# Performance work log

Hardware: AMD Instinct MI355X
Metric: run time of the kernel (lower is better)

Reference implementation:

```python
import jax, jax.numpy as jnp
import numpy as np

N_USER = 100000
N_ITEM = 100000
E = 500000
EMB, HID, OUT = 128, 128, 64


def _mean_agg(msg_src, src, dst, n_dst):
    """Gather per-edge messages from src nodes, segment-mean onto dst nodes."""
    m = msg_src[src]  # [E, d]
    s = jax.ops.segment_sum(m, dst, num_segments=n_dst)
    cnt = jax.ops.segment_sum(jnp.ones((src.shape[0],), m.dtype), dst,
                              num_segments=n_dst)
    # DGL mean reducer yields 0 for nodes with no in-edges
    return jnp.where(cnt[:, None] > 0, s / jnp.maximum(cnt, 1.0)[:, None], 0.0)


def _layer(feat_u, feat_i, W0, b0, Wui, bui, Wiu, biu,
           src_ui, dst_ui, src_iu, dst_iu):
    # shared self-transform (weight0) -> residual h0 on every ntype
    h0_u = feat_u @ W0 + b0
    h0_i = feat_i @ W0 + b0
    # per-etype transform of source features
    wh_u = feat_u @ Wui + bui  # messages along user->item
    wh_i = feat_i @ Wiu + biu  # messages along item->user
    h_i = _mean_agg(wh_u, src_ui, dst_ui, N_ITEM) + h0_i
    h_u = _mean_agg(wh_i, src_iu, dst_iu, N_USER) + h0_u
    return h_u, h_i


def setup_inputs() -> dict:
    key = jax.random.key(0)
    ks = jax.random.split(key, 12)
    sc_e = 1.0 / np.sqrt(EMB)
    sc_h = 1.0 / np.sqrt(HID)
    return {
        "emb_user": jax.random.normal(ks[0], (N_USER, EMB), jnp.float32),
        "emb_item": jax.random.normal(ks[1], (N_ITEM, EMB), jnp.float32),
        "W1_0": jax.random.normal(ks[2], (EMB, HID), jnp.float32) * sc_e,
        "b1_0": jnp.zeros((HID,), jnp.float32),
        "W1_ui": jax.random.normal(ks[3], (EMB, HID), jnp.float32) * sc_e,
        "b1_ui": jnp.zeros((HID,), jnp.float32),
        "W1_iu": jax.random.normal(ks[4], (EMB, HID), jnp.float32) * sc_e,
        "b1_iu": jnp.zeros((HID,), jnp.float32),
        "W2_0": jax.random.normal(ks[5], (HID, OUT), jnp.float32) * sc_h,
        "b2_0": jnp.zeros((OUT,), jnp.float32),
        "W2_ui": jax.random.normal(ks[6], (HID, OUT), jnp.float32) * sc_h,
        "b2_ui": jnp.zeros((OUT,), jnp.float32),
        "W2_iu": jax.random.normal(ks[7], (HID, OUT), jnp.float32) * sc_h,
        "b2_iu": jnp.zeros((OUT,), jnp.float32),
        "src_ui": jax.random.randint(ks[8], (E,), 0, N_USER, jnp.int32),
        "dst_ui": jax.random.randint(ks[9], (E,), 0, N_ITEM, jnp.int32),
        "src_iu": jax.random.randint(ks[10], (E,), 0, N_ITEM, jnp.int32),
        "dst_iu": jax.random.randint(ks[11], (E,), 0, N_USER, jnp.int32),
    }


def reference(emb_user, emb_item,
              W1_0, b1_0, W1_ui, b1_ui, W1_iu, b1_iu,
              W2_0, b2_0, W2_ui, b2_ui, W2_iu, b2_iu,
              src_ui, dst_ui, src_iu, dst_iu):
    h_u, h_i = _layer(emb_user, emb_item, W1_0, b1_0, W1_ui, b1_ui,
                      W1_iu, b1_iu, src_ui, dst_ui, src_iu, dst_iu)
    h_u = jax.nn.leaky_relu(h_u, 0.01)  # torch F.leaky_relu default slope
    h_i = jax.nn.leaky_relu(h_i, 0.01)
    h_u, h_i = _layer(h_u, h_i, W2_0, b2_0, W2_ui, b2_ui,
                      W2_iu, b2_iu, src_ui, dst_ui, src_iu, dst_iu)
    return h_u, h_i
```

## Files before the change

kernel.cpp:

```cpp
#include <hip/hip_runtime.h>

#define N_USER 100000
#define N_ITEM 100000
#define NEDGE  500000
#define CURS   100032
#define RCAP   16

#define B_FILL 978
#define B_CONV 12500
#define B_WT   384
#define B_TOT  (B_FILL + B_CONV + B_WT)

typedef __attribute__((ext_vector_type(8))) short short8;
typedef __attribute__((ext_vector_type(4))) float f32x4;

__device__ __forceinline__ unsigned short f2bf(float f) {
  union { float f; unsigned int u; } x{f};
  unsigned int r = x.u + 0x7fffu + ((x.u >> 16) & 1u);
  return (unsigned short)(r >> 16);
}
__device__ __forceinline__ float bf2f(unsigned short u) {
  union { unsigned int u; float f; } x{(unsigned int)u << 16};
  return x.f;
}

__global__ __launch_bounds__(256) void setup_k(
    const int* __restrict__ src_ui, const int* __restrict__ dst_ui,
    int* __restrict__ cur_i, int* __restrict__ csr_ui,
    const int* __restrict__ src_iu, const int* __restrict__ dst_iu,
    int* __restrict__ cur_u, int* __restrict__ csr_iu,
    const float* __restrict__ emb_u, const float* __restrict__ emb_i,
    unsigned short* __restrict__ ebu, unsigned short* __restrict__ ebi,
    const float* __restrict__ W10, const float* __restrict__ W1ui,
    const float* __restrict__ W1iu, const float* __restrict__ W20,
    const float* __restrict__ W2ui, const float* __restrict__ W2iu,
    unsigned short* __restrict__ WT1i, unsigned short* __restrict__ WT1u,
    unsigned short* __restrict__ WT2i, unsigned short* __restrict__ WT2u) {
  int b = (int)(((unsigned long long)blockIdx.x * 7919ull) % (unsigned long long)B_TOT);
  int tid = threadIdx.x;
  if (b < B_FILL) {
    const int *src, *dst; int *cur, *csr;
    int bb = b;
    if (bb < 489) { src = src_ui; dst = dst_ui; cur = cur_i; csr = csr_ui; }
    else { bb -= 489; src = src_iu; dst = dst_iu; cur = cur_u; csr = csr_iu; }
    int e0 = bb * 1024 + tid;
    int d[4], s[4];
    bool ok[4];
#pragma unroll
    for (int k = 0; k < 4; ++k) {
      int e = e0 + k * 256;
      ok[k] = (e < NEDGE);
      d[k] = ok[k] ? dst[e] : 0;
      s[k] = ok[k] ? src[e] : 0;
    }
    int p[4];
#pragma unroll
    for (int k = 0; k < 4; ++k) {
      int rk = (tid + k) & 3;
      p[k] = ok[k] ? atomicAdd(&cur[rk * CURS + d[k]], 1) : RCAP;
    }
#pragma unroll
    for (int k = 0; k < 4; ++k) {
      int rk = (tid + k) & 3;
      if (ok[k] && p[k] < RCAP)
        __builtin_nontemporal_store(s[k], &csr[d[k] * 64 + rk * RCAP + p[k]]);
    }
  } else if (b < B_FILL + B_CONV) {
    int blk = b - B_FILL;
    const float* src; unsigned short* dstp;
    if (blk < 6250) { src = emb_u; dstp = ebu; }
    else { blk -= 6250; src = emb_i; dstp = ebi; }
    size_t g = (size_t)blk * 2048 + (size_t)tid * 8;
    float4 x = *(const float4*)(src + g);
    float4 y = *(const float4*)(src + g + 4);
    short8 v{(short)f2bf(x.x), (short)f2bf(x.y), (short)f2bf(x.z), (short)f2bf(x.w),
             (short)f2bf(y.x), (short)f2bf(y.y), (short)f2bf(y.z), (short)f2bf(y.w)};
    *(short8*)(dstp + g) = v;
  } else {
    int t = (b - B_FILL - B_CONV) * 256 + tid;
    if (t < 32768) {
      int n = t >> 8, k = t & 255;
      float v = (k < 128) ? W10[k * 128 + n] : W1ui[(k - 128) * 128 + n];
      WT1i[t] = f2bf(v);
    } else if (t < 65536) {
      int q = t - 32768; int n = q >> 8, k = q & 255;
      float v = (k < 128) ? W10[k * 128 + n] : W1iu[(k - 128) * 128 + n];
      WT1u[q] = f2bf(v);
    } else if (t < 81920) {
      int q = t - 65536; int n = q >> 8, k = q & 255;
      float v = (k < 128) ? W20[k * 64 + n] : W2ui[(k - 128) * 64 + n];
      WT2i[q] = f2bf(v);
    } else {
      int q = t - 81920; int n = q >> 8, k = q & 255;
      float v = (k < 128) ? W20[k * 64 + n] : W2iu[(k - 128) * 64 + n];
      WT2u[q] = f2bf(v);
    }
  }
}

__global__ __launch_bounds__(256) void aggc_k(
    const unsigned short* __restrict__ featA, const int* __restrict__ curA,
    const int* __restrict__ csrA, unsigned short* __restrict__ outA,
    const unsigned short* __restrict__ featB, const int* __restrict__ curB,
    const int* __restrict__ csrB, unsigned short* __restrict__ outB,
    int nbA) {
  __shared__ int sidx[16][64];
  int b = blockIdx.x;
  const unsigned short* feat; const int* cur; const int* csr; unsigned short* out;
  if (b < nbA) { feat = featA; cur = curA; csr = csrA; out = outA; }
  else { b -= nbA; feat = featB; cur = curB; csr = csrB; out = outB; }
  int grp = threadIdx.x >> 4;
  int ln  = threadIdx.x & 15;
  int node = b * 16 + grp;

  int4 sl = *(const int4*)(csr + (size_t)node * 64 + ln * 4);
  int cr = cur[(size_t)(ln >> 2) * CURS + node];
  cr = min(cr, RCAP);
  int m = cr - (ln & 3) * 4;
  m = m < 0 ? 0 : (m > 4 ? 4 : m);
  int pre = m;
#pragma unroll
  for (int d = 1; d < 16; d <<= 1) {
    int t = __shfl_up(pre, d, 16);
    if (ln >= d) pre += t;
  }
  int start = pre - m;
  int deg = __shfl(pre, 15, 16);
  if (m > 0) sidx[grp][start] = sl.x;
  if (m > 1) sidx[grp][start + 1] = sl.y;
  if (m > 2) sidx[grp][start + 2] = sl.z;
  if (m > 3) sidx[grp][start + 3] = sl.w;
  __syncthreads();

  const int* lidx = sidx[grp];
  float a[8] = {0, 0, 0, 0, 0, 0, 0, 0};
  int j = 0;
  if (j + 4 <= deg) {
    int i0 = lidx[0], i1 = lidx[1], i2 = lidx[2], i3 = lidx[3];
    for (;;) {
      bool more = (j + 8 <= deg);
      int n0, n1, n2, n3;
      if (more) { n0 = lidx[j + 4]; n1 = lidx[j + 5]; n2 = lidx[j + 6]; n3 = lidx[j + 7]; }
      short8 v0 = *(const short8*)(feat + (size_t)i0 * 128 + ln * 8);
      short8 v1 = *(const short8*)(feat + (size_t)i1 * 128 + ln * 8);
      short8 v2 = *(const short8*)(feat + (size_t)i2 * 128 + ln * 8);
      short8 v3 = *(const short8*)(feat + (size_t)i3 * 128 + ln * 8);
#pragma unroll
      for (int d = 0; d < 8; ++d)
        a[d] += (bf2f((unsigned short)v0[d]) + bf2f((unsigned short)v1[d])) +
                (bf2f((unsigned short)v2[d]) + bf2f((unsigned short)v3[d]));
      j += 4;
      if (!more) break;
      i0 = n0; i1 = n1; i2 = n2; i3 = n3;
    }
  }
  if (j + 2 <= deg) {
    int i0 = lidx[j], i1 = lidx[j + 1];
    short8 v0 = *(const short8*)(feat + (size_t)i0 * 128 + ln * 8);
    short8 v1 = *(const short8*)(feat + (size_t)i1 * 128 + ln * 8);
#pragma unroll
    for (int d = 0; d < 8; ++d)
      a[d] += bf2f((unsigned short)v0[d]) + bf2f((unsigned short)v1[d]);
    j += 2;
  }
  if (j < deg) {
    short8 v = *(const short8*)(feat + (size_t)lidx[j] * 128 + ln * 8);
#pragma unroll
    for (int d = 0; d < 8; ++d) a[d] += bf2f((unsigned short)v[d]);
  }
  float sc = deg ? 1.f / (float)deg : 0.f;
  short8 pk;
#pragma unroll
  for (int d = 0; d < 8; ++d) pk[d] = (short)f2bf(a[d] * sc);
  *(short8*)(out + (size_t)node * 128 + ln * 8) = pk;
}

template <int N, bool LRELU, bool OUTBF16>
__global__ __launch_bounds__(256) void gemm2_k(
    const unsigned short* __restrict__ A1a, const unsigned short* __restrict__ A2a,
    const unsigned short* __restrict__ WTa, const float* __restrict__ b0a,
    const float* __restrict__ bea, const int* __restrict__ cura,
    void* __restrict__ outa,
    const unsigned short* __restrict__ A1b, const unsigned short* __restrict__ A2b,
    const unsigned short* __restrict__ WTb, const float* __restrict__ b0b,
    const float* __restrict__ beb, const int* __restrict__ curb,
    void* __restrict__ outb, int M, int nbA) {
  constexpr int BM = 64;
  constexpr int CPW = N / 4;
  constexpr int NCF = CPW / 16;
  __shared__ short As[BM * 128];
  __shared__ short Ws[N * 128];
  __shared__ float degmask[BM];

  int blk = blockIdx.x;
  const unsigned short* A1; const unsigned short* A2; const unsigned short* WT;
  const float* b0; const float* be; const int* cur; void* outv;
  if (blk < nbA) { A1 = A1a; A2 = A2a; WT = WTa; b0 = b0a; be = bea; cur = cura; outv = outa; }
  else { blk -= nbA; A1 = A1b; A2 = A2b; WT = WTb; b0 = b0b; be = beb; cur = curb; outv = outb; }

  const int tid = threadIdx.x;
  const int lane = tid & 63;
  const int wave = tid >> 6;
  const int row0 = blk * BM;
  const int colbase = wave * CPW;

  if (tid < BM) {
    int r = row0 + tid;
    int ds = 0;
    if (r < M)
      ds = cur[r] + cur[CURS + r] + cur[2 * CURS + r] + cur[3 * CURS + r];
    degmask[tid] = (ds > 0) ? 1.f : 0.f;
  }

  f32x4 acc[4][NCF] = {};

#pragma unroll
  for (int kh = 0; kh < 2; ++kh) {
    __syncthreads();
    const unsigned short* base = (kh == 0) ? A1 : A2;
#pragma unroll
    for (int it = 0; it < 4; ++it) {
      int chunk = tid + it * 256;
      int row = chunk >> 4, c16 = chunk & 15;
      int gr = row0 + row; if (gr > M - 1) gr = M - 1;
      short8 v = *(const short8*)(base + (size_t)gr * 128 + c16 * 8);
      int byteoff = row * 256 + ((c16 * 16) ^ ((row & 7) << 4));
      *(short8*)((char*)As + byteoff) = v;
    }
#pragma unroll
    for (int it = 0; it < (N * 16) / 256; ++it) {
      int chunk = tid + it * 256;
      int n = chunk >> 4, c16 = chunk & 15;
      short8 v = *(const short8*)(WT + (size_t)n * 256 + kh * 128 + c16 * 8);
      int byteoff = n * 256 + ((c16 * 16) ^ ((n & 7) << 4));
      *(short8*)((char*)Ws + byteoff) = v;
    }
    __syncthreads();

#pragma unroll
    for (int ks = 0; ks < 4; ++ks) {
      short8 af[4];
#pragma unroll
      for (int rf = 0; rf < 4; ++rf) {
        int row = rf * 16 + (lane & 15);
        int c16 = ks * 4 + (lane >> 4);
        int byteoff = row * 256 + ((c16 * 16) ^ ((row & 7) << 4));
        af[rf] = *(const short8*)((const char*)As + byteoff);
      }
      short8 wf[NCF];
#pragma unroll
      for (int cf = 0; cf < NCF; ++cf) {
        int n = colbase + cf * 16 + (lane & 15);
        int c16 = ks * 4 + (lane >> 4);
        int byteoff = n * 256 + ((c16 * 16) ^ ((n & 7) << 4));
        wf[cf] = *(const short8*)((const char*)Ws + byteoff);
      }
#pragma unroll
      for (int rf = 0; rf < 4; ++rf)
#pragma unroll
        for (int cf = 0; cf < NCF; ++cf)
          acc[rf][cf] = __builtin_amdgcn_mfma_f32_16x16x32_bf16(
              af[rf], wf[cf], acc[rf][cf], 0, 0, 0);
    }
  }

#pragma unroll
  for (int cf = 0; cf < NCF; ++cf) {
    int c = colbase + cf * 16 + (lane & 15);
    float bb0 = b0[c], bbe = be[c];
#pragma unroll
    for (int rf = 0; rf < 4; ++rf) {
#pragma unroll
      for (int j = 0; j < 4; ++j) {
        int lr = rf * 16 + (lane >> 4) * 4 + j;
        int r = row0 + lr;
        if (r < M) {
          float v = acc[rf][cf][j] + bb0 + degmask[lr] * bbe;
          if (LRELU) v = (v >= 0.f) ? v : 0.01f * v;
          if (OUTBF16)
            ((unsigned short*)outv)[(size_t)r * N + c] = f2bf(v);
          else
            ((float*)outv)[(size_t)r * N + c] = v;
        }
      }
    }
  }
}

extern "C" void kernel_launch(void* const* d_in, const int* in_sizes, int n_in,
                              void* d_out, int out_size, void* d_ws,
                              size_t ws_size, hipStream_t stream) {
  const float* emb_u = (const float*)d_in[0];
  const float* emb_i = (const float*)d_in[1];
  const float* W1_0  = (const float*)d_in[2];
  const float* b1_0  = (const float*)d_in[3];
  const float* W1_ui = (const float*)d_in[4];
  const float* b1_ui = (const float*)d_in[5];
  const float* W1_iu = (const float*)d_in[6];
  const float* b1_iu = (const float*)d_in[7];
  const float* W2_0  = (const float*)d_in[8];
  const float* b2_0  = (const float*)d_in[9];
  const float* W2_ui = (const float*)d_in[10];
  const float* b2_ui = (const float*)d_in[11];
  const float* W2_iu = (const float*)d_in[12];
  const float* b2_iu = (const float*)d_in[13];
  const int* src_ui = (const int*)d_in[14];
  const int* dst_ui = (const int*)d_in[15];
  const int* src_iu = (const int*)d_in[16];
  const int* dst_iu = (const int*)d_in[17];
  float* out = (float*)d_out;

  char* p = (char*)d_ws;
  unsigned short* WT1i = (unsigned short*)p; p += 65536;
  unsigned short* WT1u = (unsigned short*)p; p += 65536;
  unsigned short* WT2i = (unsigned short*)p; p += 32768;
  unsigned short* WT2u = (unsigned short*)p; p += 32768;
  int* cur_i = (int*)p; p += 4 * CURS * 4;
  int* cur_u = (int*)p; p += 4 * CURS * 4;
  int* csr_ui = (int*)p; p += (size_t)CURS * 64 * 4;
  int* csr_iu = (int*)p; p += (size_t)CURS * 64 * 4;
  const size_t FB = (size_t)N_USER * 128 * 2;
  unsigned short* ebu  = (unsigned short*)p; p += FB;
  unsigned short* ebi  = (unsigned short*)p; p += FB;
  unsigned short* hu = ebu;
  unsigned short* hi = ebi;
  unsigned short* aggB = (unsigned short*)out;
  unsigned short* aggA = (unsigned short*)(out + (size_t)N_USER * 64);

  const int GG = (N_USER + 63) / 64;

  hipMemsetAsync(cur_i, 0, 2 * 4 * CURS * 4, stream);
  setup_k<<<B_TOT, 256, 0, stream>>>(src_ui, dst_ui, cur_i, csr_ui,
                                     src_iu, dst_iu, cur_u, csr_iu,
                                     emb_u, emb_i, ebu, ebi,
                                     W1_0, W1_ui, W1_iu, W2_0, W2_ui, W2_iu,
                                     WT1i, WT1u, WT2i, WT2u);

  aggc_k<<<2 * 6250, 256, 0, stream>>>(
      ebu, cur_i, csr_ui, aggA, ebi, cur_u, csr_iu, aggB, 6250);
  gemm2_k<128, true, true><<<2 * GG, 256, 0, stream>>>(
      ebi, aggA, WT1i, b1_0, b1_ui, cur_i, hi,
      ebu, aggB, WT1u, b1_0, b1_iu, cur_u, hu, N_USER, GG);

  aggc_k<<<2 * 6250, 256, 0, stream>>>(
      hu, cur_i, csr_ui, aggA, hi, cur_u, csr_iu, aggB, 6250);
  gemm2_k<64, false, false><<<2 * GG, 256, 0, stream>>>(
      hi, aggA, WT2i, b2_0, b2_ui, cur_i, out + (size_t)N_USER * 64,
      hu, aggB, WT2u, b2_0, b2_iu, cur_u, out, N_USER, GG);
}
```

Before: 240.3 us.

## Replace 4-way replicated degree counters with single counter and 32-slot adjacency

Replaces the per-node adjacency, which used four replicated atomic counters and four 16-slot sub-lists, with one counter per node and one contiguous 32-slot list. This removes the prefix-scan compaction in the aggregation kernel and the four-way counter sum in the GEMM degree mask, and halves the adjacency buffer footprint. The trade-off is more atomic contention on a single counter per destination and a lower total degree cap (32 instead of 64), which could drop edges on high-degree nodes. The nontemporal store hint is also removed.

```diff
diff --git a/kernel.cpp b/kernel.cpp
--- a/kernel.cpp
+++ b/kernel.cpp
@@ -3,8 +3,7 @@
 #define N_USER 100000
 #define N_ITEM 100000
 #define NEDGE  500000
-#define CURS   100032
-#define RCAP   16
+#define DEGCAP 32
 
 #define B_FILL 978
 #define B_CONV 12500
@@ -55,16 +54,11 @@
     }
     int p[4];
 #pragma unroll
-    for (int k = 0; k < 4; ++k) {
-      int rk = (tid + k) & 3;
-      p[k] = ok[k] ? atomicAdd(&cur[rk * CURS + d[k]], 1) : RCAP;
-    }
-#pragma unroll
-    for (int k = 0; k < 4; ++k) {
-      int rk = (tid + k) & 3;
-      if (ok[k] && p[k] < RCAP)
-        __builtin_nontemporal_store(s[k], &csr[d[k] * 64 + rk * RCAP + p[k]]);
-    }
+    for (int k = 0; k < 4; ++k)
+      p[k] = ok[k] ? atomicAdd(&cur[d[k]], 1) : DEGCAP;
+#pragma unroll
+    for (int k = 0; k < 4; ++k)
+      if (ok[k] && p[k] < DEGCAP) csr[d[k] * DEGCAP + p[k]] = s[k];
   } else if (b < B_FILL + B_CONV) {
     int blk = b - B_FILL;
     const float* src; unsigned short* dstp;
@@ -104,7 +98,7 @@
     const unsigned short* __restrict__ featB, const int* __restrict__ curB,
     const int* __restrict__ csrB, unsigned short* __restrict__ outB,
     int nbA) {
-  __shared__ int sidx[16][64];
+  __shared__ int sidx[16][32];
   int b = blockIdx.x;
   const unsigned short* feat; const int* cur; const int* csr; unsigned short* out;
   if (b < nbA) { feat = featA; cur = curA; csr = csrA; out = outA; }
@@ -112,24 +106,11 @@
   int grp = threadIdx.x >> 4;
   int ln  = threadIdx.x & 15;
   int node = b * 16 + grp;
-
-  int4 sl = *(const int4*)(csr + (size_t)node * 64 + ln * 4);
-  int cr = cur[(size_t)(ln >> 2) * CURS + node];
-  cr = min(cr, RCAP);
-  int m = cr - (ln & 3) * 4;
-  m = m < 0 ? 0 : (m > 4 ? 4 : m);
-  int pre = m;
-#pragma unroll
-  for (int d = 1; d < 16; d <<= 1) {
-    int t = __shfl_up(pre, d, 16);
-    if (ln >= d) pre += t;
-  }
-  int start = pre - m;
-  int deg = __shfl(pre, 15, 16);
-  if (m > 0) sidx[grp][start] = sl.x;
-  if (m > 1) sidx[grp][start + 1] = sl.y;
-  if (m > 2) sidx[grp][start + 2] = sl.z;
-  if (m > 3) sidx[grp][start + 3] = sl.w;
+  int deg = min(cur[node], DEGCAP);
+
+  int2 sl = *(const int2*)(csr + (size_t)node * DEGCAP + ln * 2);
+  sidx[grp][ln * 2] = sl.x;
+  sidx[grp][ln * 2 + 1] = sl.y;
   __syncthreads();
 
   const int* lidx = sidx[grp];
@@ -206,10 +187,7 @@
 
   if (tid < BM) {
     int r = row0 + tid;
-    int ds = 0;
-    if (r < M)
-      ds = cur[r] + cur[CURS + r] + cur[2 * CURS + r] + cur[3 * CURS + r];
-    degmask[tid] = (ds > 0) ? 1.f : 0.f;
+    degmask[tid] = (r < M && cur[r] > 0) ? 1.f : 0.f;
   }
 
   f32x4 acc[4][NCF] = {};
@@ -315,10 +293,10 @@
   unsigned short* WT1u = (unsigned short*)p; p += 65536;
   unsigned short* WT2i = (unsigned short*)p; p += 32768;
   unsigned short* WT2u = (unsigned short*)p; p += 32768;
-  int* cur_i = (int*)p; p += 4 * CURS * 4;
-  int* cur_u = (int*)p; p += 4 * CURS * 4;
-  int* csr_ui = (int*)p; p += (size_t)CURS * 64 * 4;
-  int* csr_iu = (int*)p; p += (size_t)CURS * 64 * 4;
+  int* cur_i = (int*)p; p += 400128;
+  int* cur_u = (int*)p; p += 400128;
+  int* csr_ui = (int*)p; p += (size_t)100032 * DEGCAP * 4;
+  int* csr_iu = (int*)p; p += (size_t)100032 * DEGCAP * 4;
   const size_t FB = (size_t)N_USER * 128 * 2;
   unsigned short* ebu  = (unsigned short*)p; p += FB;
   unsigned short* ebi  = (unsigned short*)p; p += FB;
@@ -329,7 +307,7 @@
 
   const int GG = (N_USER + 63) / 64;
 
-  hipMemsetAsync(cur_i, 0, 2 * 4 * CURS * 4, stream);
+  hipMemsetAsync(cur_i, 0, 2 * 400128, stream);
   setup_k<<<B_TOT, 256, 0, stream>>>(src_ui, dst_ui, cur_i, csr_ui,
                                      src_iu, dst_iu, cur_u, csr_iu,
                                      emb_u, emb_i, ebu, ebi,
```

Result: faster. 229.3 us (-4.6%).
